# Performance work log

Hardware: AMD Instinct MI355X
Metric: run time of the kernel (lower is better)

Reference implementation:

```python
import jax, jax.numpy as jnp
import numpy as np

H = 2048      # hidden_size
I = 8192      # intermediate_size
NH = 16       # num_heads
HD = H // NH  # head_dim
EPS = 1e-6


def setup_inputs() -> dict:
    key = jax.random.key(0)
    ks = jax.random.split(key, 10)
    s = 0.02
    return {
        "hidden_states": jax.random.normal(ks[0], (2, 2048, H), dtype=jnp.float32),
        "wq": jax.random.normal(ks[1], (H, H), dtype=jnp.float32) * s,
        "wk": jax.random.normal(ks[2], (H, H), dtype=jnp.float32) * s,
        "wv": jax.random.normal(ks[3], (H, H), dtype=jnp.float32) * s,
        "wo": jax.random.normal(ks[4], (H, H), dtype=jnp.float32) * s,
        "w_gate": jax.random.normal(ks[5], (H, I), dtype=jnp.float32) * s,
        "w_up": jax.random.normal(ks[6], (H, I), dtype=jnp.float32) * s,
        "w_down": jax.random.normal(ks[7], (I, H), dtype=jnp.float32) * s,
        "ln1_w": jnp.ones((H,), dtype=jnp.float32),
        "ln2_w": jnp.ones((H,), dtype=jnp.float32),
    }


def rmsnorm(x, w):
    xf = x.astype(jnp.float32)
    var = jnp.mean(xf * xf, axis=-1, keepdims=True)
    return w * (xf * jax.lax.rsqrt(var + EPS)).astype(x.dtype)


def reference(hidden_states, wq, wk, wv, wo, w_gate, w_up, w_down, ln1_w, ln2_w):
    b, s, _ = hidden_states.shape
    residual = hidden_states
    x = rmsnorm(hidden_states, ln1_w)

    # attention (no RoPE, no causal mask, per source)
    q = (x @ wq).reshape(b, s, NH, HD)
    k = (x @ wk).reshape(b, s, NH, HD)
    v = (x @ wv).reshape(b, s, NH, HD)
    scores = jnp.einsum('bqhd,bkhd->bhqk', q, k) / jnp.sqrt(jnp.float32(HD))
    attn = jax.nn.softmax(scores, axis=-1)
    out = jnp.einsum('bhqk,bkhd->bqhd', attn, v).reshape(b, s, H)
    hidden = residual + out @ wo

    residual = hidden
    y = rmsnorm(hidden, ln2_w)
    gate = jax.nn.silu(y @ w_gate)
    up = y @ w_up
    return residual + (gate * up) @ w_down
```

## Files before the change

### kernel.cpp

```cpp
#include <hip/hip_runtime.h>
#include <hip/hip_bf16.h>

#define HDIM 2048
#define IDIM 8192
#define NHEADS 16
#define HEADD 128
#define BATCH 2
#define SEQ 2048
#define MTOK 4096

typedef unsigned short u16;
typedef __bf16 bf16x8 __attribute__((ext_vector_type(8)));
typedef float f32x4 __attribute__((ext_vector_type(4)));
typedef float f32x16 __attribute__((ext_vector_type(16)));
typedef unsigned short u16x8 __attribute__((ext_vector_type(8)));
typedef unsigned int u32x2 __attribute__((ext_vector_type(2)));
typedef unsigned int u32x4 __attribute__((ext_vector_type(4)));
typedef unsigned int uv2 __attribute__((ext_vector_type(2)));

__device__ __forceinline__ u16 f2b(float f) {
  unsigned u = __builtin_bit_cast(unsigned, f);
  u += 0x7FFFu + ((u >> 16) & 1u);
  return (u16)(u >> 16);
}
__device__ __forceinline__ float b2f(u16 b) {
  unsigned u = ((unsigned)b) << 16;
  return __builtin_bit_cast(float, u);
}
__device__ __forceinline__ void gl_lds16(const void* g, void* l) {
  auto gp = (const __attribute__((address_space(1))) unsigned int*)((unsigned long long)g);
  auto lp = (__attribute__((address_space(3))) unsigned int*)((unsigned)(unsigned long long)l);
  __builtin_amdgcn_global_load_lds(gp, lp, 16, 0, 0);
}
__device__ __forceinline__ unsigned cvtpk(float lo, float hi) {
  unsigned r;
  asm("v_cvt_pk_bf16_f32 %0, %1, %2" : "=v"(r) : "v"(lo), "v"(hi));
  return r;
}
__device__ __forceinline__ void rect_swz(int gx, int gy, int& bx, int& by) {
  const int bid = blockIdx.y * gx + blockIdx.x;
  const int xcd = bid & 7, ii = bid >> 3;
  const int j = ii & 31, rin = ii >> 5;
  const int rectIdx = rin * 8 + xcd;
  const int nry = gy >> 2;
  const int ry = rectIdx % nry, rx = rectIdx / nry;
  by = ry * 4 + (j >> 3);
  bx = rx * 8 + (j & 7);
}

__global__ __launch_bounds__(256) void wtrans_all(const float* __restrict__ wq, const float* __restrict__ wk,
                                                  const float* __restrict__ wv, const float* __restrict__ wo,
                                                  const float* __restrict__ wg, const float* __restrict__ wu,
                                                  const float* __restrict__ wd,
                                                  u16* __restrict__ wqkvT, u16* __restrict__ woT,
                                                  u16* __restrict__ wgT, u16* __restrict__ wuT,
                                                  u16* __restrict__ wdT) {
  int bidf = blockIdx.x;
  const float* W;
  u16* Wt;
  int K, N, rowoff, bx, by;
  if (bidf < 3072) {
    int s = bidf >> 10, r = bidf & 1023;
    W = s == 0 ? wq : (s == 1 ? wk : wv);
    Wt = wqkvT; K = 2048; N = 2048; rowoff = s * 2048;
    bx = r & 31; by = r >> 5;
  } else if (bidf < 4096) {
    int r = bidf - 3072;
    W = wo; Wt = woT; K = 2048; N = 2048; rowoff = 0;
    bx = r & 31; by = r >> 5;
  } else if (bidf < 8192) {
    int r = bidf - 4096;
    W = wg; Wt = wgT; K = 2048; N = 8192; rowoff = 0;
    bx = r & 127; by = r >> 7;
  } else if (bidf < 12288) {
    int r = bidf - 8192;
    W = wu; Wt = wuT; K = 2048; N = 8192; rowoff = 0;
    bx = r & 127; by = r >> 7;
  } else {
    int r = bidf - 12288;
    W = wd; Wt = wdT; K = 8192; N = 2048; rowoff = 0;
    bx = r & 31; by = r >> 5;
  }
  __shared__ float t[64][65];
  int n0 = bx * 64, k0 = by * 64;
  int tid = threadIdx.x;
  int kr = tid >> 4, nc = (tid & 15) * 4;
#pragma unroll
  for (int p = 0; p < 4; p++) {
    float4 v = *(const float4*)&W[(size_t)(k0 + p * 16 + kr) * N + n0 + nc];
    t[nc + 0][p * 16 + kr] = v.x;
    t[nc + 1][p * 16 + kr] = v.y;
    t[nc + 2][p * 16 + kr] = v.z;
    t[nc + 3][p * 16 + kr] = v.w;
  }
  __syncthreads();
  int n = tid >> 2, kq = (tid & 3) * 16;
  u16 tmp[16];
#pragma unroll
  for (int i = 0; i < 16; i++) tmp[i] = f2b(t[n][kq + i]);
  *(u16x8*)&Wt[(size_t)(rowoff + n0 + n) * K + k0 + kq] = *(u16x8*)&tmp[0];
  *(u16x8*)&Wt[(size_t)(rowoff + n0 + n) * K + k0 + kq + 8] = *(u16x8*)&tmp[8];
}

__global__ __launch_bounds__(256) void vtrans_k(const u16* __restrict__ qkv, u16* __restrict__ vt) {
  __shared__ u16 t[32][33];
  int s0 = blockIdx.x * 32, d0 = blockIdx.y * 32, bh = blockIdx.z;
  int b = bh >> 4, h = bh & 15;
  int tx = threadIdx.x, ty = threadIdx.y;
#pragma unroll
  for (int i = 0; i < 4; i++)
    t[ty + i * 8][tx] = qkv[(size_t)(b * SEQ + s0 + ty + i * 8) * 6144 + 4096 + h * HEADD + d0 + tx];
  __syncthreads();
#pragma unroll
  for (int i = 0; i < 4; i++)
    vt[(size_t)(bh * HEADD + d0 + ty + i * 8) * SEQ + s0 + tx] = t[tx][ty + i * 8];
}

__global__ __launch_bounds__(256) void rmsnorm_k(const float* __restrict__ X, const float* __restrict__ W,
                                                 u16* __restrict__ O) {
  int row = blockIdx.x;
  int tid = threadIdx.x;
  const float* x = X + (size_t)row * HDIM;
  float4 v0 = ((const float4*)x)[tid * 2];
  float4 v1 = ((const float4*)x)[tid * 2 + 1];
  float ss = v0.x * v0.x + v0.y * v0.y + v0.z * v0.z + v0.w * v0.w
           + v1.x * v1.x + v1.y * v1.y + v1.z * v1.z + v1.w * v1.w;
#pragma unroll
  for (int off = 32; off > 0; off >>= 1) ss += __shfl_down(ss, off);
  __shared__ float red[4];
  if ((tid & 63) == 0) red[tid >> 6] = ss;
  __syncthreads();
  float rs = rsqrtf((red[0] + red[1] + red[2] + red[3]) * (1.0f / HDIM) + 1e-6f);
  const float* w = W + tid * 8;
  u16* o = O + (size_t)row * HDIM + tid * 8;
  float vals[8] = {v0.x, v0.y, v0.z, v0.w, v1.x, v1.y, v1.z, v1.w};
#pragma unroll
  for (int j = 0; j < 8; j++) o[j] = f2b(w[j] * vals[j] * rs);
}

template <int EPI>
__global__ __launch_bounds__(512, 2) void gemm_lean(const u16* __restrict__ A, const u16* __restrict__ Bt,
                                                    int M, int N, int K,
                                                    u16* __restrict__ Cb, float* __restrict__ Cf,
                                                    const float* __restrict__ Res) {
  __shared__ char lds[147456];
  const int tid = threadIdx.x, lane = tid & 63, w = tid >> 6;
  const int wm = w >> 1, wn = w & 1;
  int bx, by;
  rect_swz(gridDim.x, gridDim.y, bx, by);
  const int m0 = by * 256, n0 = bx * 128;
  const int NT = K >> 6;

  const int srow = w * 8 + (lane >> 3);
  const int kko = ((lane & 7) ^ (lane >> 3)) * 8;
  const u16* Asrc = A + (size_t)(m0 + srow) * K + kko;
  const u16* Bsrc = Bt + (size_t)(n0 + srow) * K + kko;
  const int wofs = w * 1024;

#define SSA(buf, kt)                                                                          \
  {                                                                                           \
    gl_lds16(Asrc + (size_t)(kt) * 64, lds + (buf) * 49152 + wofs);                           \
    gl_lds16(Asrc + 64 * (size_t)K + (size_t)(kt) * 64, lds + (buf) * 49152 + 8192 + wofs);   \
    gl_lds16(Asrc + 128 * (size_t)K + (size_t)(kt) * 64, lds + (buf) * 49152 + 16384 + wofs); \
    gl_lds16(Asrc + 192 * (size_t)K + (size_t)(kt) * 64, lds + (buf) * 49152 + 24576 + wofs); \
  }
#define SSB(buf, kt)                                                                         \
  {                                                                                          \
    gl_lds16(Bsrc + (size_t)(kt) * 64, lds + (buf) * 49152 + 32768 + wofs);                  \
    gl_lds16(Bsrc + 64 * (size_t)K + (size_t)(kt) * 64, lds + (buf) * 49152 + 40960 + wofs); \
  }
#define LG0 { asm volatile("s_waitcnt lgkmcnt(0)" ::: "memory"); __builtin_amdgcn_sched_barrier(0); }

  const int l15 = lane & 15, l4 = lane >> 4;
  const int kq0 = ((l4) ^ (l15 & 7)) << 4;
  const int kq1 = ((4 + l4) ^ (l15 & 7)) << 4;
  const int abase = (wm * 64 + l15) * 128;
  const int bbase = 32768 + (wn * 64 + l15) * 128;

  const f32x4 fz = {0.f, 0.f, 0.f, 0.f};
  f32x4 acc[4][4];
#pragma unroll
  for (int i = 0; i < 4; i++)
#pragma unroll
    for (int jj = 0; jj < 4; jj++) acc[i][jj] = fz;
  bf16x8 af0[4], af1[4], b0[4], b1[4];

  SSA(0, 0);
  SSB(0, 0);
  {
    const int t1p = (1 < NT) ? 1 : 0;
    SSA(1, t1p);
    SSB(1, t1p);
  }
  asm volatile("s_waitcnt vmcnt(6)" ::: "memory");
  __builtin_amdgcn_s_barrier();

  for (int t = 0; t < NT; ++t) {
    const int bt = t % 3, bs = (t + 2) % 3;
    const char* Lb = lds + bt * 49152;
    const int t2 = (t + 2 < NT) ? t + 2 : NT - 1;
#pragma unroll
    for (int mf = 0; mf < 4; mf++) af0[mf] = *(const bf16x8*)(Lb + abase + mf * 2048 + kq0);
#pragma unroll
    for (int nf = 0; nf < 4; nf++) b0[nf] = *(const bf16x8*)(Lb + bbase + nf * 2048 + kq0);
    SSA(bs, t2);
    SSB(bs, t2);
    LG0;
    __builtin_amdgcn_s_setprio(1);
#pragma unroll
    for (int mf = 0; mf < 4; mf++)
#pragma unroll
      for (int nf = 0; nf < 4; nf++)
        acc[mf][nf] = __builtin_amdgcn_mfma_f32_16x16x32_bf16(af0[mf], b0[nf], acc[mf][nf], 0, 0, 0);
    __builtin_amdgcn_s_setprio(0);
#pragma unroll
    for (int mf = 0; mf < 4; mf++) af1[mf] = *(const bf16x8*)(Lb + abase + mf * 2048 + kq1);
#pragma unroll
    for (int nf = 0; nf < 4; nf++) b1[nf] = *(const bf16x8*)(Lb + bbase + nf * 2048 + kq1);
    LG0;
    __builtin_amdgcn_s_setprio(1);
#pragma unroll
    for (int mf = 0; mf < 4; mf++)
#pragma unroll
      for (int nf = 0; nf < 4; nf++)
        acc[mf][nf] = __builtin_amdgcn_mfma_f32_16x16x32_bf16(af1[mf], b1[nf], acc[mf][nf], 0, 0, 0);
    __builtin_amdgcn_s_setprio(0);
    asm volatile("s_waitcnt vmcnt(6)" ::: "memory");
    __builtin_amdgcn_s_barrier();
  }
  asm volatile("s_waitcnt vmcnt(0)" ::: "memory");

#pragma unroll
  for (int mf = 0; mf < 4; mf++) {
#pragma unroll
    for (int jr = 0; jr < 4; jr++) {
      const int m = m0 + wm * 64 + mf * 16 + l4 * 4 + jr;
#pragma unroll
      for (int nf = 0; nf < 4; nf++) {
        const int n = n0 + wn * 64 + nf * 16 + l15;
        float v = acc[mf][nf][jr];
        size_t idx = (size_t)m * N + n;
        if (EPI == 0) {
          Cb[idx] = f2b(v);
        } else {
          Cf[idx] = Res[idx] + v;
        }
      }
    }
  }
#undef SSA
#undef SSB
#undef LG0
}

__global__ __launch_bounds__(512, 2) void gemm_fgu2(const u16* __restrict__ A, const u16* __restrict__ Bg,
                                                    const u16* __restrict__ Bu, u16* __restrict__ G) {
  __shared__ char lds[131072];
  const int tid = threadIdx.x, lane = tid & 63, w = tid >> 6;
  const int wm = w >> 2, wn = w & 3;
  int bx, by;
  rect_swz(64, 16, bx, by);
  const int m0 = by * 256, n0 = bx * 128;
  const int NT = 32;

  const int srow = w * 8 + (lane >> 3);
  const int kko = ((lane & 7) ^ (lane >> 3)) * 8;
  const u16* Asrc = A + (size_t)(m0 + srow) * 2048 + kko;
  const u16* Bgsrc = Bg + (size_t)(n0 + srow) * 2048 + kko;
  const u16* Busrc = Bu + (size_t)(n0 + srow) * 2048 + kko;
  const int wofs = w * 1024;

#define SSA(buf, kt)                                                              \
  {                                                                               \
    gl_lds16(Asrc + (kt) * 64, lds + (buf) * 65536 + wofs);                       \
    gl_lds16(Asrc + 64 * 2048 + (kt) * 64, lds + (buf) * 65536 + 8192 + wofs);    \
    gl_lds16(Asrc + 128 * 2048 + (kt) * 64, lds + (buf) * 65536 + 16384 + wofs);  \
    gl_lds16(Asrc + 192 * 2048 + (kt) * 64, lds + (buf) * 65536 + 24576 + wofs);  \
  }
#define SBGU(buf, kt)                                                             \
  {                                                                               \
    gl_lds16(Bgsrc + (kt) * 64, lds + (buf) * 65536 + 32768 + wofs);              \
    gl_lds16(Bgsrc + 64 * 2048 + (kt) * 64, lds + (buf) * 65536 + 40960 + wofs);  \
    gl_lds16(Busrc + (kt) * 64, lds + (buf) * 65536 + 49152 + wofs);              \
    gl_lds16(Busrc + 64 * 2048 + (kt) * 64, lds + (buf) * 65536 + 57344 + wofs);  \
  }
#define LG0 { asm volatile("s_waitcnt lgkmcnt(0)" ::: "memory"); __builtin_amdgcn_sched_barrier(0); }

  const int l15 = lane & 15, l4 = lane >> 4;
  const int kq0 = ((l4) ^ (l15 & 7)) << 4;
  const int kq1 = ((4 + l4) ^ (l15 & 7)) << 4;
  const int abase = (wm * 128 + l15) * 128;
  const int gbase = 32768 + (wn * 32 + l15) * 128;
  const int ubase = 49152 + (wn * 32 + l15) * 128;

  const f32x4 fz = {0.f, 0.f, 0.f, 0.f};
  f32x4 ag[8][2], au[8][2];
#pragma unroll
  for (int i = 0; i < 8; i++)
#pragma unroll
    for (int jj = 0; jj < 2; jj++) { ag[i][jj] = fz; au[i][jj] = fz; }
  bf16x8 af0[8], af1[8], bg0[2], bg1[2], bu0[2], bu1[2];

  SSA(0, 0);
  SBGU(0, 0);
  asm volatile("s_waitcnt vmcnt(4)" ::: "memory");
  __builtin_amdgcn_s_barrier();

  for (int t = 0; t < NT; ++t) {
    const int buf = t & 1, nb = buf ^ 1;
    const char* Lb = lds + buf * 65536;
    const int t1 = (t + 1 < NT) ? t + 1 : NT - 1;
#pragma unroll
    for (int mf = 0; mf < 8; mf++) af0[mf] = *(const bf16x8*)(Lb + abase + mf * 2048 + kq0);
    SSA(nb, t1);
    asm volatile("s_waitcnt vmcnt(4)" ::: "memory");
    __builtin_amdgcn_s_barrier();
    bg0[0] = *(const bf16x8*)(Lb + gbase + kq0);
    bg0[1] = *(const bf16x8*)(Lb + gbase + 2048 + kq0);
    bu0[0] = *(const bf16x8*)(Lb + ubase + kq0);
    bu0[1] = *(const bf16x8*)(Lb + ubase + 2048 + kq0);
    bg1[0] = *(const bf16x8*)(Lb + gbase + kq1);
    bg1[1] = *(const bf16x8*)(Lb + gbase + 2048 + kq1);
    bu1[0] = *(const bf16x8*)(Lb + ubase + kq1);
    bu1[1] = *(const bf16x8*)(Lb + ubase + 2048 + kq1);
    LG0;
    __builtin_amdgcn_s_setprio(1);
#pragma unroll
    for (int mf = 0; mf < 8; mf++) {
      ag[mf][0] = __builtin_amdgcn_mfma_f32_16x16x32_bf16(af0[mf], bg0[0], ag[mf][0], 0, 0, 0);
      ag[mf][1] = __builtin_amdgcn_mfma_f32_16x16x32_bf16(af0[mf], bg0[1], ag[mf][1], 0, 0, 0);
      au[mf][0] = __builtin_amdgcn_mfma_f32_16x16x32_bf16(af0[mf], bu0[0], au[mf][0], 0, 0, 0);
      au[mf][1] = __builtin_amdgcn_mfma_f32_16x16x32_bf16(af0[mf], bu0[1], au[mf][1], 0, 0, 0);
    }
    __builtin_amdgcn_s_setprio(0);
#pragma unroll
    for (int mf = 0; mf < 8; mf++) af1[mf] = *(const bf16x8*)(Lb + abase + mf * 2048 + kq1);
    SBGU(nb, t1);
    asm volatile("s_waitcnt vmcnt(4)" ::: "memory");
    LG0;
    __builtin_amdgcn_s_barrier();
    __builtin_amdgcn_s_setprio(1);
#pragma unroll
    for (int mf = 0; mf < 8; mf++) {
      ag[mf][0] = __builtin_amdgcn_mfma_f32_16x16x32_bf16(af1[mf], bg1[0], ag[mf][0], 0, 0, 0);
      ag[mf][1] = __builtin_amdgcn_mfma_f32_16x16x32_bf16(af1[mf], bg1[1], ag[mf][1], 0, 0, 0);
      au[mf][0] = __builtin_amdgcn_mfma_f32_16x16x32_bf16(af1[mf], bu1[0], au[mf][0], 0, 0, 0);
      au[mf][1] = __builtin_amdgcn_mfma_f32_16x16x32_bf16(af1[mf], bu1[1], au[mf][1], 0, 0, 0);
    }
    __builtin_amdgcn_s_setprio(0);
  }
  asm volatile("s_waitcnt vmcnt(0)" ::: "memory");

#pragma unroll
  for (int mf = 0; mf < 8; mf++) {
#pragma unroll
    for (int jr = 0; jr < 4; jr++) {
      const int m = m0 + wm * 128 + mf * 16 + l4 * 4 + jr;
#pragma unroll
      for (int nf = 0; nf < 2; nf++) {
        const int n = n0 + wn * 32 + nf * 16 + l15;
        float g = ag[mf][nf][jr];
        float u = au[mf][nf][jr];
        float sg = g / (1.f + __expf(-g));
        G[(size_t)m * IDIM + n] = f2b(sg * u);
      }
    }
  }
#undef SSA
#undef SBGU
#undef LG0
}

__global__ __launch_bounds__(512, 2) void attn_k(const u16* __restrict__ qkv, const u16* __restrict__ vt,
                                                 u16* __restrict__ out) {
  __shared__ char Kl[2][16384];
  __shared__ char Vl[2][16384];
  int tid = threadIdx.x, lane = tid & 63, w = tid >> 6;
  int bid = blockIdx.y * 8 + blockIdx.x;
  int swz = (bid & 7) * 32 + (bid >> 3);
  int qb = swz & 7, bh = swz >> 3;
  int b = bh >> 4, h = bh & 15;
  int l31 = lane & 31, hi = lane >> 5;
  const float c = 0.088388347648318447f * 1.4426950408889634f;
  const float RT = 90.51f;

  const int qrow = qb * 256 + w * 32 + l31;
  bf16x8 q[8];
  {
    const u16* qp = qkv + (size_t)(b * SEQ + qrow) * 6144 + h * HEADD + hi * 8;
#pragma unroll
    for (int dt = 0; dt < 8; dt++) q[dt] = *(const bf16x8*)(qp + dt * 16);
  }
  f32x16 o[4];
#pragma unroll
  for (int i = 0; i < 4; i++)
#pragma unroll
    for (int j = 0; j < 16; j++) o[i][j] = 0.f;
  float mrow = -1e30f, lrow = 0.f;

#define ASTAGE(buf, t)                                                                     \
  {                                                                                        \
    int kv0_ = (t) * 64;                                                                   \
    _Pragma("unroll") for (int i = 0; i < 2; i++) {                                        \
      int r = w * 8 + i * 4 + (lane >> 4);                                                 \
      int col = ((lane & 15) ^ (r & 15)) * 8;                                              \
      const u16* src = qkv + (size_t)(b * SEQ + kv0_ + r) * 6144 + HDIM + h * HEADD + col; \
      gl_lds16(src, &Kl[buf][(w * 8 + i * 4) * 256]);                                      \
    }                                                                                      \
    _Pragma("unroll") for (int i = 0; i < 2; i++) {                                        \
      int d = w * 16 + i * 8 + (lane >> 3);                                                \
      int col = ((lane & 7) ^ (d & 7)) * 8;                                                \
      const u16* src = vt + (size_t)(bh * HEADD + d) * SEQ + kv0_ + col;                   \
      gl_lds16(src, &Vl[buf][(w * 16 + i * 8) * 128]);                                     \
    }                                                                                      \
  }

  ASTAGE(0, 0);
  __syncthreads();

  for (int t = 0; t < SEQ / 64; t++) {
    const int buf = t & 1;
    if (t + 1 < SEQ / 64) ASTAGE(buf ^ 1, t + 1);
    const char* Kb = &Kl[buf][0];
    const char* Vb = &Vl[buf][0];
    f32x16 s0, s1;
#pragma unroll
    for (int j = 0; j < 16; j++) { s0[j] = 0.f; s1[j] = 0.f; }
    const int ksl = l31 & 15;
    __builtin_amdgcn_s_setprio(1);
#pragma unroll
    for (int dt = 0; dt < 8; dt++) {
      bf16x8 k0 = *(const bf16x8*)(Kb + (l31)*256 + (((dt * 2 + hi) ^ ksl) << 4));
      bf16x8 k1 = *(const bf16x8*)(Kb + (32 + l31) * 256 + (((dt * 2 + hi) ^ ksl) << 4));
      s0 = __builtin_amdgcn_mfma_f32_32x32x16_bf16(k0, q[dt], s0, 0, 0, 0);
      s1 = __builtin_amdgcn_mfma_f32_32x32x16_bf16(k1, q[dt], s1, 0, 0, 0);
    }
    __builtin_amdgcn_s_setprio(0);
    float m8[8];
#pragma unroll
    for (int g = 0; g < 4; g++) {
      m8[g] = fmaxf(fmaxf(s0[4 * g], s0[4 * g + 1]), fmaxf(s0[4 * g + 2], s0[4 * g + 3]));
      m8[4 + g] = fmaxf(fmaxf(s1[4 * g], s1[4 * g + 1]), fmaxf(s1[4 * g + 2], s1[4 * g + 3]));
    }
    float vmax = fmaxf(fmaxf(fmaxf(m8[0], m8[1]), fmaxf(m8[2], m8[3])),
                       fmaxf(fmaxf(m8[4], m8[5]), fmaxf(m8[6], m8[7])));
    {
      uv2 pr = __builtin_amdgcn_permlane32_swap(__builtin_bit_cast(unsigned, vmax),
                                                __builtin_bit_cast(unsigned, vmax), false, false);
      vmax = fmaxf(__builtin_bit_cast(float, pr[0]), __builtin_bit_cast(float, pr[1]));
    }
    if (__any(vmax > mrow + RT)) {
      float mnew = fmaxf(mrow, vmax);
      float alpha = exp2f((mrow - mnew) * c);
      mrow = mnew;
      lrow *= alpha;
#pragma unroll
      for (int i = 0; i < 4; i++)
#pragma unroll
        for (int j = 0; j < 16; j++) o[i][j] *= alpha;
    }
    const float mc = mrow * c;
    float r4[4] = {0.f, 0.f, 0.f, 0.f};
#pragma unroll
    for (int j = 0; j < 16; j++) {
      s0[j] = exp2f(s0[j] * c - mc);
      r4[j & 3] += s0[j];
    }
#pragma unroll
    for (int j = 0; j < 16; j++) {
      s1[j] = exp2f(s1[j] * c - mc);
      r4[j & 3] += s1[j];
    }
    float rsum = (r4[0] + r4[1]) + (r4[2] + r4[3]);
    {
      uv2 pr = __builtin_amdgcn_permlane32_swap(__builtin_bit_cast(unsigned, rsum),
                                                __builtin_bit_cast(unsigned, rsum), false, false);
      rsum = __builtin_bit_cast(float, pr[0]) + __builtin_bit_cast(float, pr[1]);
    }
    lrow += rsum;
    bf16x8 pa[4];
#pragma unroll
    for (int half = 0; half < 2; half++) {
      const f32x16& sv = half ? s1 : s0;
#pragma unroll
      for (int blk = 0; blk < 2; blk++) {
        int base = blk * 8;
        unsigned A = cvtpk(sv[base + 0], sv[base + 1]);
        unsigned B = cvtpk(sv[base + 2], sv[base + 3]);
        unsigned C = cvtpk(sv[base + 4], sv[base + 5]);
        unsigned D = cvtpk(sv[base + 6], sv[base + 7]);
        uv2 ac = __builtin_amdgcn_permlane32_swap(A, C, false, false);
        uv2 bd = __builtin_amdgcn_permlane32_swap(B, D, false, false);
        u32x4 w4;
        w4[0] = ac[0]; w4[1] = bd[0]; w4[2] = ac[1]; w4[3] = bd[1];
        pa[half * 2 + blk] = __builtin_bit_cast(bf16x8, w4);
      }
    }
    __builtin_amdgcn_s_setprio(1);
#pragma unroll
    for (int dt4 = 0; dt4 < 4; dt4++) {
      const char* vbase = Vb + (dt4 * 32 + l31) * 128;
      const int vsl = l31 & 7;
#pragma unroll
      for (int ks = 0; ks < 4; ks++) {
        bf16x8 vb = *(const bf16x8*)(vbase + (((ks * 2 + hi) ^ vsl) << 4));
        o[dt4] = __builtin_amdgcn_mfma_f32_32x32x16_bf16(vb, pa[ks], o[dt4], 0, 0, 0);
      }
    }
    __builtin_amdgcn_s_setprio(0);
    __syncthreads();
  }
#undef ASTAGE

  const float linv = 1.0f / lrow;
  u16* orow = out + (size_t)(b * SEQ + qrow) * HDIM + h * HEADD;
#pragma unroll
  for (int dt4 = 0; dt4 < 4; dt4++) {
#pragma unroll
    for (int g = 0; g < 4; g++) {
      u32x2 st;
      st[0] = cvtpk(o[dt4][4 * g + 0] * linv, o[dt4][4 * g + 1] * linv);
      st[1] = cvtpk(o[dt4][4 * g + 2] * linv, o[dt4][4 * g + 3] * linv);
      *(u32x2*)(orow + dt4 * 32 + 8 * g + 4 * hi) = st;
    }
  }
}

extern "C" void kernel_launch(void* const* d_in, const int* in_sizes, int n_in,
                              void* d_out, int out_size, void* d_ws, size_t ws_size,
                              hipStream_t stream) {
  const float* hs  = (const float*)d_in[0];
  const float* wq  = (const float*)d_in[1];
  const float* wk  = (const float*)d_in[2];
  const float* wv  = (const float*)d_in[3];
  const float* wo  = (const float*)d_in[4];
  const float* wg  = (const float*)d_in[5];
  const float* wu  = (const float*)d_in[6];
  const float* wd  = (const float*)d_in[7];
  const float* ln1 = (const float*)d_in[8];
  const float* ln2 = (const float*)d_in[9];
  char* ws = (char*)d_ws;
  u16*   wqkvT = (u16*)(ws);
  u16*   woT   = (u16*)(ws + 25165824ull);
  u16*   wgT   = (u16*)(ws + 33554432ull);
  u16*   wuT   = (u16*)(ws + 67108864ull);
  u16*   wdT   = (u16*)(ws + 100663296ull);
  u16*   xb    = (u16*)(ws + 134217728ull);
  float* hid   = (float*)(ws + 150994944ull);
  u16*   qkv   = (u16*)(ws + 184549376ull);
  u16*   vtb   = (u16*)(ws + 234881024ull);
  u16*   attn  = (u16*)(ws + 251658368ull);
  u16*   g     = qkv;

  wtrans_all<<<16384, 256, 0, stream>>>(wq, wk, wv, wo, wg, wu, wd, wqkvT, woT, wgT, wuT, wdT);

  rmsnorm_k<<<MTOK, 256, 0, stream>>>(hs, ln1, xb);
  gemm_lean<0><<<dim3(48, 16), 512, 0, stream>>>(xb, wqkvT, MTOK, 6144, HDIM, qkv, nullptr, nullptr);
  vtrans_k<<<dim3(64, 4, 32), dim3(32, 8), 0, stream>>>(qkv, vtb);
  attn_k<<<dim3(8, 32), 512, 0, stream>>>(qkv, vtb, attn);
  gemm_lean<3><<<dim3(16, 16), 512, 0, stream>>>(attn, woT, MTOK, HDIM, HDIM, nullptr, hid, hs);
  rmsnorm_k<<<MTOK, 256, 0, stream>>>(hid, ln2, xb);
  gemm_fgu2<<<dim3(64, 16), 512, 0, stream>>>(xb, wgT, wuT, g);
  gemm_lean<3><<<dim3(16, 16), 512, 0, stream>>>(g, wdT, MTOK, HDIM, IDIM, nullptr, (float*)d_out, hid);
}
```

Before: 700.4 us.

## Triple-buffer A and double-buffer B in gate/up GEMM with one barrier per step

Restructures the fused gate/up GEMM's LDS pipeline. The A tiles now use three buffers and the gate/up B tiles use two separate buffers, so loads for step t+1 (B) and t+2 (A) are issued before the MFMAs of step t. This drops the two mid-iteration barriers and waits down to a single vmcnt wait and barrier at the end of each k-step. The aim is to hide global-to-LDS latency better and cut synchronization stalls. The cost is that LDS per block grows to 160KB, which uses the CU's full LDS and still allows only one block per CU.

```diff
diff --git a/kernel.cpp b/kernel.cpp
--- a/kernel.cpp
+++ b/kernel.cpp
@@ -253,9 +253,9 @@
 #undef LG0
 }
 
-__global__ __launch_bounds__(512, 2) void gemm_fgu2(const u16* __restrict__ A, const u16* __restrict__ Bg,
+__global__ __launch_bounds__(512, 2) void gemm_fgu4(const u16* __restrict__ A, const u16* __restrict__ Bg,
                                                     const u16* __restrict__ Bu, u16* __restrict__ G) {
-  __shared__ char lds[131072];
+  __shared__ char lds[163840];
   const int tid = threadIdx.x, lane = tid & 63, w = tid >> 6;
   const int wm = w >> 2, wn = w & 3;
   int bx, by;
@@ -270,19 +270,19 @@
   const u16* Busrc = Bu + (size_t)(n0 + srow) * 2048 + kko;
   const int wofs = w * 1024;
 
-#define SSA(buf, kt)                                                              \
-  {                                                                               \
-    gl_lds16(Asrc + (kt) * 64, lds + (buf) * 65536 + wofs);                       \
-    gl_lds16(Asrc + 64 * 2048 + (kt) * 64, lds + (buf) * 65536 + 8192 + wofs);    \
-    gl_lds16(Asrc + 128 * 2048 + (kt) * 64, lds + (buf) * 65536 + 16384 + wofs);  \
-    gl_lds16(Asrc + 192 * 2048 + (kt) * 64, lds + (buf) * 65536 + 24576 + wofs);  \
-  }
-#define SBGU(buf, kt)                                                             \
-  {                                                                               \
-    gl_lds16(Bgsrc + (kt) * 64, lds + (buf) * 65536 + 32768 + wofs);              \
-    gl_lds16(Bgsrc + 64 * 2048 + (kt) * 64, lds + (buf) * 65536 + 40960 + wofs);  \
-    gl_lds16(Busrc + (kt) * 64, lds + (buf) * 65536 + 49152 + wofs);              \
-    gl_lds16(Busrc + 64 * 2048 + (kt) * 64, lds + (buf) * 65536 + 57344 + wofs);  \
+#define SSA(buf, kt)                                                                  \
+  {                                                                                   \
+    gl_lds16(Asrc + (kt) * 64, lds + (buf) * 32768 + wofs);                           \
+    gl_lds16(Asrc + 64 * 2048 + (kt) * 64, lds + (buf) * 32768 + 8192 + wofs);        \
+    gl_lds16(Asrc + 128 * 2048 + (kt) * 64, lds + (buf) * 32768 + 16384 + wofs);      \
+    gl_lds16(Asrc + 192 * 2048 + (kt) * 64, lds + (buf) * 32768 + 24576 + wofs);      \
+  }
+#define SBGU(buf, kt)                                                                    \
+  {                                                                                      \
+    gl_lds16(Bgsrc + (kt) * 64, lds + 98304 + (buf) * 32768 + wofs);                     \
+    gl_lds16(Bgsrc + 64 * 2048 + (kt) * 64, lds + 98304 + (buf) * 32768 + 8192 + wofs);  \
+    gl_lds16(Busrc + (kt) * 64, lds + 98304 + (buf) * 32768 + 16384 + wofs);             \
+    gl_lds16(Busrc + 64 * 2048 + (kt) * 64, lds + 98304 + (buf) * 32768 + 24576 + wofs); \
   }
 #define LG0 { asm volatile("s_waitcnt lgkmcnt(0)" ::: "memory"); __builtin_amdgcn_sched_barrier(0); }
 
@@ -290,8 +290,7 @@
   const int kq0 = ((l4) ^ (l15 & 7)) << 4;
   const int kq1 = ((4 + l4) ^ (l15 & 7)) << 4;
   const int abase = (wm * 128 + l15) * 128;
-  const int gbase = 32768 + (wn * 32 + l15) * 128;
-  const int ubase = 49152 + (wn * 32 + l15) * 128;
+  const int gofs = (wn * 32 + l15) * 128;
 
   const f32x4 fz = {0.f, 0.f, 0.f, 0.f};
   f32x4 ag[8][2], au[8][2];
@@ -301,28 +300,26 @@
     for (int jj = 0; jj < 2; jj++) { ag[i][jj] = fz; au[i][jj] = fz; }
   bf16x8 af0[8], af1[8], bg0[2], bg1[2], bu0[2], bu1[2];
 
+  SBGU(0, 0);
   SSA(0, 0);
-  SBGU(0, 0);
+  SSA(1, 1);
   asm volatile("s_waitcnt vmcnt(4)" ::: "memory");
   __builtin_amdgcn_s_barrier();
 
   for (int t = 0; t < NT; ++t) {
-    const int buf = t & 1, nb = buf ^ 1;
-    const char* Lb = lds + buf * 65536;
+    const int ab = t % 3, bb = t & 1;
+    const char* La = lds + ab * 32768;
+    const char* Lbg = lds + 98304 + bb * 32768;
     const int t1 = (t + 1 < NT) ? t + 1 : NT - 1;
-#pragma unroll
-    for (int mf = 0; mf < 8; mf++) af0[mf] = *(const bf16x8*)(Lb + abase + mf * 2048 + kq0);
-    SSA(nb, t1);
-    asm volatile("s_waitcnt vmcnt(4)" ::: "memory");
-    __builtin_amdgcn_s_barrier();
-    bg0[0] = *(const bf16x8*)(Lb + gbase + kq0);
-    bg0[1] = *(const bf16x8*)(Lb + gbase + 2048 + kq0);
-    bu0[0] = *(const bf16x8*)(Lb + ubase + kq0);
-    bu0[1] = *(const bf16x8*)(Lb + ubase + 2048 + kq0);
-    bg1[0] = *(const bf16x8*)(Lb + gbase + kq1);
-    bg1[1] = *(const bf16x8*)(Lb + gbase + 2048 + kq1);
-    bu1[0] = *(const bf16x8*)(Lb + ubase + kq1);
-    bu1[1] = *(const bf16x8*)(Lb + ubase + 2048 + kq1);
+    const int t2 = (t + 2 < NT) ? t + 2 : NT - 1;
+#pragma unroll
+    for (int mf = 0; mf < 8; mf++) af0[mf] = *(const bf16x8*)(La + abase + mf * 2048 + kq0);
+    bg0[0] = *(const bf16x8*)(Lbg + gofs + kq0);
+    bg0[1] = *(const bf16x8*)(Lbg + gofs + 2048 + kq0);
+    bu0[0] = *(const bf16x8*)(Lbg + 16384 + gofs + kq0);
+    bu0[1] = *(const bf16x8*)(Lbg + 16384 + gofs + 2048 + kq0);
+    SBGU((t + 1) & 1, t1);
+    SSA((t + 2) % 3, t2);
     LG0;
     __builtin_amdgcn_s_setprio(1);
 #pragma unroll
@@ -334,11 +331,12 @@
     }
     __builtin_amdgcn_s_setprio(0);
 #pragma unroll
-    for (int mf = 0; mf < 8; mf++) af1[mf] = *(const bf16x8*)(Lb + abase + mf * 2048 + kq1);
-    SBGU(nb, t1);
-    asm volatile("s_waitcnt vmcnt(4)" ::: "memory");
+    for (int mf = 0; mf < 8; mf++) af1[mf] = *(const bf16x8*)(La + abase + mf * 2048 + kq1);
+    bg1[0] = *(const bf16x8*)(Lbg + gofs + kq1);
+    bg1[1] = *(const bf16x8*)(Lbg + gofs + 2048 + kq1);
+    bu1[0] = *(const bf16x8*)(Lbg + 16384 + gofs + kq1);
+    bu1[1] = *(const bf16x8*)(Lbg + 16384 + gofs + 2048 + kq1);
     LG0;
-    __builtin_amdgcn_s_barrier();
     __builtin_amdgcn_s_setprio(1);
 #pragma unroll
     for (int mf = 0; mf < 8; mf++) {
@@ -348,6 +346,8 @@
       au[mf][1] = __builtin_amdgcn_mfma_f32_16x16x32_bf16(af1[mf], bu1[1], au[mf][1], 0, 0, 0);
     }
     __builtin_amdgcn_s_setprio(0);
+    asm volatile("s_waitcnt vmcnt(4)" ::: "memory");
+    __builtin_amdgcn_s_barrier();
   }
   asm volatile("s_waitcnt vmcnt(0)" ::: "memory");
 
@@ -560,6 +560,6 @@
   attn_k<<<dim3(8, 32), 512, 0, stream>>>(qkv, vtb, attn);
   gemm_lean<3><<<dim3(16, 16), 512, 0, stream>>>(attn, woT, MTOK, HDIM, HDIM, nullptr, hid, hs);
   rmsnorm_k<<<MTOK, 256, 0, stream>>>(hid, ln2, xb);
-  gemm_fgu2<<<dim3(64, 16), 512, 0, stream>>>(xb, wgT, wuT, g);
+  gemm_fgu4<<<dim3(64, 16), 512, 0, stream>>>(xb, wgT, wuT, g);
   gemm_lean<3><<<dim3(16, 16), 512, 0, stream>>>(g, wdT, MTOK, HDIM, IDIM, nullptr, (float*)d_out, hid);
 }
```

After: 713.7 us. No clear change (+1.9%).

## Add dedicated QKV GEMM computing Q, K, V tiles together to reuse A tiles

Applied to the files above, without the earlier changes.

Replaces the generic 48x16-block QKV projection GEMM with a specialized 1024-thread kernel. Each block loads one 256-row A tile and the matching 128-column slices of Wq, Wk and Wv, so A is read from global memory once instead of three times. Grid shrinks to 256 blocks with one block per CU and a larger LDS footprint. The risk is lower occupancy and fewer blocks than CUs on MI355X, which can leave some CUs idle, plus higher register pressure from 24 accumulators per thread.

```diff
diff --git a/kernel.cpp b/kernel.cpp
--- a/kernel.cpp
+++ b/kernel.cpp
@@ -138,6 +138,122 @@
   for (int j = 0; j < 8; j++) o[j] = f2b(w[j] * vals[j] * rs);
 }
 
+__global__ __launch_bounds__(1024, 1) void gemm_q3(const u16* __restrict__ A, const u16* __restrict__ Bqkv,
+                                                   u16* __restrict__ Out) {
+  __shared__ char lds[163840];
+  const int tid = threadIdx.x, lane = tid & 63, w = tid >> 6;
+  const int wm = w >> 2, wn = w & 3;
+  int bx, by;
+  rect_swz(16, 16, bx, by);
+  const int m0 = by * 256, n0 = bx * 128;
+  const int NT = 32;
+
+  const int srow = w * 8 + (lane >> 3);
+  const int kko = ((lane & 7) ^ (lane >> 3)) * 8;
+  const u16* Asrc = A + (size_t)(m0 + srow) * 2048 + kko;
+  const u16* B0src = Bqkv + (size_t)(n0 + srow) * 2048 + kko;
+  const u16* B1src = Bqkv + (size_t)(2048 + n0 + srow) * 2048 + kko;
+  const u16* B2src = Bqkv + (size_t)(4096 + n0 + srow) * 2048 + kko;
+  const int wofs = w * 1024;
+
+#define SSA(buf, kt)                                                              \
+  {                                                                               \
+    gl_lds16(Asrc + (kt) * 64, lds + (buf) * 32768 + wofs);                       \
+    gl_lds16(Asrc + 128 * 2048 + (kt) * 64, lds + (buf) * 32768 + 16384 + wofs);  \
+  }
+#define SSB(buf, kt)                                                              \
+  {                                                                               \
+    gl_lds16(B0src + (kt) * 64, lds + 65536 + (buf) * 49152 + wofs);              \
+    gl_lds16(B1src + (kt) * 64, lds + 65536 + (buf) * 49152 + 16384 + wofs);      \
+    gl_lds16(B2src + (kt) * 64, lds + 65536 + (buf) * 49152 + 32768 + wofs);      \
+  }
+#define LG0 { asm volatile("s_waitcnt lgkmcnt(0)" ::: "memory"); __builtin_amdgcn_sched_barrier(0); }
+
+  const int l15 = lane & 15, l4 = lane >> 4;
+  const int kq0 = ((l4) ^ (l15 & 7)) << 4;
+  const int kq1 = ((4 + l4) ^ (l15 & 7)) << 4;
+  const int abase = (wm >> 1) * 16384 + ((wm & 1) * 64 + l15) * 128;
+  const int bbase = (wn * 32 + l15) * 128;
+
+  const f32x4 fz = {0.f, 0.f, 0.f, 0.f};
+  f32x4 acc[3][4][2];
+#pragma unroll
+  for (int i = 0; i < 3; i++)
+#pragma unroll
+    for (int mf = 0; mf < 4; mf++) { acc[i][mf][0] = fz; acc[i][mf][1] = fz; }
+  bf16x8 af0[4], af1[4], b[3][2][2];
+
+  SSA(0, 0);
+  SSB(0, 0);
+  asm volatile("s_waitcnt vmcnt(3)" ::: "memory");
+  __builtin_amdgcn_s_barrier();
+
+  for (int t = 0; t < NT; ++t) {
+    const int buf = t & 1, nb = buf ^ 1;
+    const char* La = lds + buf * 32768;
+    const char* LbB = lds + 65536 + buf * 49152;
+    const int t1 = (t + 1 < NT) ? t + 1 : NT - 1;
+#pragma unroll
+    for (int mf = 0; mf < 4; mf++) af0[mf] = *(const bf16x8*)(La + abase + mf * 2048 + kq0);
+    SSA(nb, t1);
+    asm volatile("s_waitcnt vmcnt(2)" ::: "memory");
+    __builtin_amdgcn_s_barrier();
+#pragma unroll
+    for (int i = 0; i < 3; i++) {
+#pragma unroll
+      for (int nf = 0; nf < 2; nf++) {
+        b[i][nf][0] = *(const bf16x8*)(LbB + i * 16384 + bbase + nf * 2048 + kq0);
+        b[i][nf][1] = *(const bf16x8*)(LbB + i * 16384 + bbase + nf * 2048 + kq1);
+      }
+    }
+    LG0;
+    __builtin_amdgcn_s_setprio(1);
+#pragma unroll
+    for (int i = 0; i < 3; i++)
+#pragma unroll
+      for (int mf = 0; mf < 4; mf++) {
+        acc[i][mf][0] = __builtin_amdgcn_mfma_f32_16x16x32_bf16(af0[mf], b[i][0][0], acc[i][mf][0], 0, 0, 0);
+        acc[i][mf][1] = __builtin_amdgcn_mfma_f32_16x16x32_bf16(af0[mf], b[i][1][0], acc[i][mf][1], 0, 0, 0);
+      }
+    __builtin_amdgcn_s_setprio(0);
+#pragma unroll
+    for (int mf = 0; mf < 4; mf++) af1[mf] = *(const bf16x8*)(La + abase + mf * 2048 + kq1);
+    SSB(nb, t1);
+    asm volatile("s_waitcnt vmcnt(3)" ::: "memory");
+    LG0;
+    __builtin_amdgcn_s_barrier();
+    __builtin_amdgcn_s_setprio(1);
+#pragma unroll
+    for (int i = 0; i < 3; i++)
+#pragma unroll
+      for (int mf = 0; mf < 4; mf++) {
+        acc[i][mf][0] = __builtin_amdgcn_mfma_f32_16x16x32_bf16(af1[mf], b[i][0][1], acc[i][mf][0], 0, 0, 0);
+        acc[i][mf][1] = __builtin_amdgcn_mfma_f32_16x16x32_bf16(af1[mf], b[i][1][1], acc[i][mf][1], 0, 0, 0);
+      }
+    __builtin_amdgcn_s_setprio(0);
+  }
+  asm volatile("s_waitcnt vmcnt(0)" ::: "memory");
+
+#pragma unroll
+  for (int i = 0; i < 3; i++) {
+#pragma unroll
+    for (int mf = 0; mf < 4; mf++) {
+#pragma unroll
+      for (int jr = 0; jr < 4; jr++) {
+        const int m = m0 + wm * 64 + mf * 16 + l4 * 4 + jr;
+#pragma unroll
+        for (int nf = 0; nf < 2; nf++) {
+          const int n = i * 2048 + n0 + wn * 32 + nf * 16 + l15;
+          Out[(size_t)m * 6144 + n] = f2b(acc[i][mf][nf][jr]);
+        }
+      }
+    }
+  }
+#undef SSA
+#undef SSB
+#undef LG0
+}
+
 template <int EPI>
 __global__ __launch_bounds__(512, 2) void gemm_lean(const u16* __restrict__ A, const u16* __restrict__ Bt,
                                                     int M, int N, int K,
@@ -555,7 +671,7 @@
   wtrans_all<<<16384, 256, 0, stream>>>(wq, wk, wv, wo, wg, wu, wd, wqkvT, woT, wgT, wuT, wdT);
 
   rmsnorm_k<<<MTOK, 256, 0, stream>>>(hs, ln1, xb);
-  gemm_lean<0><<<dim3(48, 16), 512, 0, stream>>>(xb, wqkvT, MTOK, 6144, HDIM, qkv, nullptr, nullptr);
+  gemm_q3<<<dim3(16, 16), 1024, 0, stream>>>(xb, wqkvT, qkv);
   vtrans_k<<<dim3(64, 4, 32), dim3(32, 8), 0, stream>>>(qkv, vtb);
   attn_k<<<dim3(8, 32), 512, 0, stream>>>(qkv, vtb, attn);
   gemm_lean<3><<<dim3(16, 16), 512, 0, stream>>>(attn, woT, MTOK, HDIM, HDIM, nullptr, hid, hs);
```

Result: slower. 1.473 ms (+110.3%).
